# Kernel tuning notes

Hardware: AMD Instinct MI355X
Metric: run time of the kernel (lower is better)

Reference implementation:

```python
import math
import jax, jax.numpy as jnp
import numpy as np
from jax import lax

N_HEADS = 8
FACTOR = 5


def _pos_emb(L, d):
    pos = jnp.arange(L, dtype=jnp.float32)[:, None]
    div = jnp.exp(jnp.arange(0, d, 2, dtype=jnp.float32) * (-math.log(10000.0) / d))
    pe = jnp.zeros((L, d), jnp.float32)
    pe = pe.at[:, 0::2].set(jnp.sin(pos * div))
    pe = pe.at[:, 1::2].set(jnp.cos(pos * div))
    return pe


def _circ_conv1d(x, w, b=None):
    # x: (B, L, Cin); w: torch conv1d weight (Cout, Cin, 3); circular padding=1
    xp = jnp.concatenate([x[:, -1:], x, x[:, :1]], axis=1)
    y = lax.conv_general_dilated(xp, jnp.transpose(w, (2, 1, 0)), (1,), 'VALID',
                                 dimension_numbers=('NWC', 'WIO', 'NWC'))
    return y + b if b is not None else y


def _ln(x, g, b, eps=1e-5):
    mu = x.mean(-1, keepdims=True)
    var = ((x - mu) ** 2).mean(-1, keepdims=True)
    return (x - mu) * lax.rsqrt(var + eps) * g + b


def _prob_attn(q, k, v, key):
    # q,k,v: (b, h, L, d); self-attention so l_q == l_k == L
    b, h, L, d = q.shape
    u = min(L, int(FACTOR * math.log(L + 1)))  # sample_k == n_top
    idx = jnp.asarray(jax.random.randint(key, (L, u), 0, L))  # shared across b,h as in torch

    # sampled QK scores: scan over the u samples to avoid a (b,h,L,u,d) gather blow-up
    def step(_, idx_s):
        kg = k[:, :, idx_s]  # (b,h,L,d): key idx_s[l] for query l
        return None, jnp.einsum('bhld,bhld->bhl', q, kg)
    _, qk = lax.scan(step, None, idx.T)  # (u, b, h, L)
    qk = jnp.moveaxis(qk, 0, -1)  # (b, h, L, u)

    m = qk.max(axis=-1) - qk.mean(axis=-1)  # sparsity measure, (b,h,L)
    _, top = lax.top_k(m, u)  # (b,h,u) top-u query indices

    q_red = jnp.take_along_axis(q, top[..., None], axis=2)  # (b,h,u,d)
    scores = jnp.einsum('bhud,bhkd->bhuk', q_red, k) * (1.0 / math.sqrt(d))
    attn = jax.nn.softmax(scores, axis=-1)
    ctx_top = jnp.einsum('bhuk,bhkd->bhud', attn, v)

    # non-selected queries get mean(V); scatter sparse-attention rows back in
    ctx = jnp.broadcast_to(v.mean(axis=2, keepdims=True), (b, h, L, d))
    bi = jnp.arange(b)[:, None, None]
    hi = jnp.arange(h)[None, :, None]
    return ctx.at[bi, hi, top].set(ctx_top)


def _attn_layer(x, wq, bq, wk, bk, wv, bv, wo, bo, key):
    b, L, dm = x.shape
    dh = dm // N_HEADS
    def split(w_, b_):
        return (x @ w_.T + b_).reshape(b, L, N_HEADS, dh).transpose(0, 2, 1, 3)
    ctx = _prob_attn(split(wq, bq), split(wk, bk), split(wv, bv), key)
    ctx = ctx.transpose(0, 2, 1, 3).reshape(b, L, dm)
    return ctx @ wo.T + bo


def _conv_layer(x, w, b, g, beta):
    # circular conv -> BatchNorm (batch stats, train-mode math) -> ELU -> maxpool k3 s2 p1
    y = _circ_conv1d(x, w, b)
    mu = y.mean(axis=(0, 1))
    var = y.var(axis=(0, 1))
    y = (y - mu) * lax.rsqrt(var + 1e-5) * g + beta
    y = jax.nn.elu(y)
    yp = jnp.pad(y, ((0, 0), (1, 1), (0, 0)), constant_values=-np.inf)
    return lax.reduce_window(yp, -np.inf, lax.max, (1, 3, 1), (1, 2, 1), 'VALID')


def _forward(x, skip_w, skip_b, token_conv_w, wq, bq, wk, bk, wv, bv, wo, bo,
             w1, b1, w2, b2, ln1_g, ln1_b, ln2_g, ln2_b,
             dc_w, dc_b, bn_g, bn_b, final_ln_g, final_ln_b, proj_w, proj_b):
    skip = x[:, -1] @ skip_w.T + skip_b  # (B, pred_len)
    h = _circ_conv1d(x, token_conv_w)  # token embedding (no bias)
    h = h + _pos_emb(h.shape[1], h.shape[2])
    E = wq.shape[0]
    base = jax.random.key(42)
    for i in range(E):
        new_h = _attn_layer(h, wq[i], bq[i], wk[i], bk[i], wv[i], bv[i], wo[i], bo[i],
                            jax.random.fold_in(base, i))
        h = h + new_h
        y = _ln(h, ln1_g[i], ln1_b[i])
        y = jax.nn.gelu(y @ w1[i].T + b1[i], approximate=False)  # conv1 is 1x1
        y = y @ w2[i].T + b2[i]  # conv2 is 1x1
        h = _ln(h + y, ln2_g[i], ln2_b[i])
        if i < E - 1:
            h = _conv_layer(h, dc_w[i], dc_b[i], bn_g[i], bn_b[i])  # halves L
    h = _ln(h, final_ln_g, final_ln_b)
    return h[:, -1] @ proj_w.T + proj_b + skip


def setup_inputs() -> dict:
    B, L, C_IN, D, DFF, E, P = 32, 2048, 7, 512, 2048, 3, 96
    key = jax.random.key(0)
    ks = iter(jax.random.split(key, 20))
    w = lambda shape: jax.random.normal(next(ks), shape, jnp.float32) * 0.02
    z = lambda shape: jnp.zeros(shape, jnp.float32)
    o = lambda shape: jnp.ones(shape, jnp.float32)
    return {
        'x': jax.random.normal(next(ks), (B, L, C_IN), jnp.float32),
        'skip_w': w((P, C_IN)), 'skip_b': z((P,)),
        'token_conv_w': w((D, C_IN, 3)),
        'wq': w((E, D, D)), 'bq': z((E, D)),
        'wk': w((E, D, D)), 'bk': z((E, D)),
        'wv': w((E, D, D)), 'bv': z((E, D)),
        'wo': w((E, D, D)), 'bo': z((E, D)),
        'w1': w((E, DFF, D)), 'b1': z((E, DFF)),
        'w2': w((E, D, DFF)), 'b2': z((E, D)),
        'ln1_g': o((E, D)), 'ln1_b': z((E, D)),
        'ln2_g': o((E, D)), 'ln2_b': z((E, D)),
        'dc_w': w((E - 1, D, D, 3)), 'dc_b': z((E - 1, D)),
        'bn_g': o((E - 1, D)), 'bn_b': z((E - 1, D)),
        'final_ln_g': o((D,)), 'final_ln_b': z((D,)),
        'proj_w': w((P, D)), 'proj_b': z((P,)),
    }


def reference(x, skip_w, skip_b, token_conv_w, wq, bq, wk, bk, wv, bv, wo, bo,
              w1, b1, w2, b2, ln1_g, ln1_b, ln2_g, ln2_b,
              dc_w, dc_b, bn_g, bn_b, final_ln_g, final_ln_b, proj_w, proj_b):
    return _forward(x, skip_w, skip_b, token_conv_w, wq, bq, wk, bk, wv, bv, wo, bo,
                    w1, b1, w2, b2, ln1_g, ln1_b, ln2_g, ln2_b,
                    dc_w, dc_b, bn_g, bn_b, final_ln_g, final_ln_b, proj_w, proj_b)
```

## Files before the change

### kernel.cpp

```cpp
#include <hip/hip_runtime.h>
#include <cmath>

#define DM 512
#define DH 64

typedef __attribute__((ext_vector_type(8))) short short8;
typedef __attribute__((ext_vector_type(4))) float float4v;

__device__ inline float b2f(unsigned short u){
  union{unsigned int i; float f;} z; z.i = ((unsigned)u)<<16; return z.f;
}
__device__ inline unsigned short f2b(float f){
  unsigned int x = __float_as_uint(f);
  return (unsigned short)((x + 0x7fffu + ((x>>16)&1u)) >> 16);
}

#define GLL(gp, lp) __builtin_amdgcn_global_load_lds((const __attribute__((address_space(1))) void*)(gp), \
    (__attribute__((address_space(3))) void*)(lp), 16, 0, 0)

__host__ __device__ inline void tf2x32(unsigned k0, unsigned k1, unsigned& x0, unsigned& x1){
  const unsigned ks0=k0, ks1=k1, ks2=k0^k1^0x1BD11BDAu;
  x0 += ks0; x1 += ks1;
#define TF_ROT(r) { x0 += x1; x1 = (x1<<(r))|(x1>>(32-(r))); x1 ^= x0; }
  TF_ROT(13) TF_ROT(15) TF_ROT(26) TF_ROT(6)
  x0 += ks1; x1 += ks2 + 1u;
  TF_ROT(17) TF_ROT(29) TF_ROT(16) TF_ROT(24)
  x0 += ks2; x1 += ks0 + 2u;
  TF_ROT(13) TF_ROT(15) TF_ROT(26) TF_ROT(6)
  x0 += ks0; x1 += ks1 + 3u;
  TF_ROT(17) TF_ROT(29) TF_ROT(16) TF_ROT(24)
  x0 += ks1; x1 += ks2 + 4u;
  TF_ROT(13) TF_ROT(15) TF_ROT(26) TF_ROT(6)
  x0 += ks2; x1 += ks0 + 5u;
#undef TF_ROT
}

__global__ __launch_bounds__(256) void idx_kernel(int* __restrict__ idx, unsigned k2a, unsigned k2b,
                                                  int S2, int Lmask){
  int j = blockIdx.x*256 + threadIdx.x;
  if (j >= S2) return;
  unsigned x0 = (unsigned)j, x1 = (unsigned)(S2 + j);
  tf2x32(k2a, k2b, x0, x1);
  idx[j]      = (int)(x0 & (unsigned)Lmask);
  idx[S2 + j] = (int)(x1 & (unsigned)Lmask);
}

__global__ __launch_bounds__(256) void pe_kernel(float* __restrict__ pe, int L){
  int i = blockIdx.x*256 + threadIdx.x;
  int d = i % DM, l = i / DM;
  const float scale = -0.017988946f;
  float freq = expf((float)(d & ~1) * scale);
  float ang  = (float)l * freq;
  pe[i] = (d & 1) ? cosf(ang) : sinf(ang);
}

__global__ __launch_bounds__(256) void packtcw(const float* __restrict__ tcw, float* __restrict__ tcwT){
  int i = blockIdx.x*256 + threadIdx.x;
  if (i >= 21*DM) return;
  int j = i / DM, d = i % DM;
  tcwT[(size_t)j*DM + d] = tcw[(size_t)d*21 + (j%7)*3 + (j/7)];
}

__global__ __launch_bounds__(256) void embed2(const float* __restrict__ x, const float* __restrict__ tcwT,
                                              const float* __restrict__ pe, float* __restrict__ h, int L){
  int row = blockIdx.x; int l = row % L, b = row / L;
  __shared__ float xs[21];
  int t = threadIdx.x;
  if (t < 21){
    int c = t % 7, kk = t / 7;
    int ls = l + kk - 1; ls = (ls < 0) ? ls + L : (ls >= L ? ls - L : ls);
    xs[t] = x[((size_t)b*L + ls)*7 + c];
  }
  __syncthreads();
  for (int d = t; d < DM; d += 256){
    float acc = 0.f;
#pragma unroll
    for (int j=0;j<21;j++) acc += xs[j]*tcwT[j*DM + d];
    h[(size_t)row*DM + d] = acc + pe[(size_t)l*DM + d];
  }
}

__global__ __launch_bounds__(256) void f2b_vec(const float* __restrict__ src, unsigned short* __restrict__ dst, int n4){
  int i = blockIdx.x*256 + threadIdx.x;
  if (i >= n4) return;
  float4 v = ((const float4*)src)[i];
  ushort4 o; o.x = f2b(v.x); o.y = f2b(v.y); o.z = f2b(v.z); o.w = f2b(v.w);
  ((ushort4*)dst)[i] = o;
}

__global__ __launch_bounds__(256) void packconv(const float* __restrict__ dcw, unsigned short* __restrict__ wtapK){
  int i = blockIdx.x*256 + threadIdx.x;
  if (i >= 3*DM*DM) return;
  int n = i / (3*DM); int rem = i % (3*DM); int tap = rem / DM; int c = rem % DM;
  wtapK[(size_t)n*(3*DM) + tap*DM + c] = f2b(dcw[((size_t)n*DM + c)*3 + tap]);
}

__global__ __launch_bounds__(256) void catb_kernel(const float* __restrict__ a, const float* __restrict__ b,
    const float* __restrict__ c, float* __restrict__ o){
  int i = blockIdx.x*256 + threadIdx.x;
  if (i >= 1536) return;
  o[i] = (i < 512) ? a[i] : (i < 1024 ? b[i-512] : c[i-1024]);
}

template<int TN, int A32>
__global__ __launch_bounds__(256) void bgemm2(const void* __restrict__ Ain,
    const unsigned short* __restrict__ Wb, const float* __restrict__ bias, void* __restrict__ C,
    int N, int K, int L, int convmode, int act, int outbf, int qkv, size_t bufstride, int swz){
  constexpr int NJ = TN/32;
  constexpr int BR = TN/32;
  __shared__ unsigned short As[128*64];
  __shared__ unsigned short Bs[TN*64];
  int tid = threadIdx.x;
  int w = tid >> 6, ln = tid & 63;

  int bx = blockIdx.x, by = blockIdx.y;
  if (swz){
    int XT = gridDim.x, YT = gridDim.y;
    int lid = by*XT + bx;
    int xcd = lid & 7, s = lid >> 3;
    int ych = YT >> 3;
    int CHv = ych < 16 ? ych : 16;
    int yloc = s % CHv;
    int t2 = s / CHv;
    int xx = t2 % XT;
    int chunk = t2 / XT;
    by = xcd*ych + chunk*CHv + yloc;
    bx = xx;
  }
  int row0 = by*128, col0 = bx*TN;
  int KA = convmode ? 512 : K;

  long aBase[4], dPrev[4], dNext[4]; int aCol[4];
#pragma unroll
  for (int g=0; g<4; g++){
    int ch = g*256 + tid;
    int r = ch >> 3, c = ch & 7;
    int gc = c ^ (r & 7);
    int gr = row0 + r;
    aCol[g] = gc*8;
    aBase[g] = (long)gr * KA;
    if (convmode){
      int l = gr % L;
      dPrev[g] = (l==0)   ? (long)(L-1)*KA : -(long)KA;
      dNext[g] = (l==L-1) ? -(long)(L-1)*KA : (long)KA;
    } else { dPrev[g]=0; dNext[g]=0; }
  }
  long bBase[BR];
#pragma unroll
  for (int g=0; g<BR; g++){
    int ch = g*256 + tid;
    int r = ch >> 3, c = ch & 7;
    int gc = c ^ (r & 7);
    bBase[g] = (long)(col0 + r)*K + gc*8;
  }
  int raBase[4], rbBase[NJ];
#pragma unroll
  for (int i=0;i<4;i++)  raBase[i] = ((w&1)*64 + i*16 + (ln&15))*8;
#pragma unroll
  for (int j=0;j<NJ;j++) rbBase[j] = ((w>>1)*(TN/2) + j*16 + (ln&15))*8;

  float4v acc[4][NJ] = {};
  int nIter = K/64;
  const unsigned short* A16 = (const unsigned short*)Ain;
  const float* Af = (const float*)Ain;

  for (int it=0; it<nIter; it++){
    int k0 = it*64;
    int kk = convmode ? (k0 & 511) : k0;
    int seg = convmode ? (k0 >> 9) : 1;
    if (A32){
#pragma unroll
      for (int g=0; g<4; g++){
        long d = convmode ? ((seg==0) ? dPrev[g] : (seg==2 ? dNext[g] : 0)) : 0;
        const float* src = Af + aBase[g] + d + kk + aCol[g];
        float4 v0 = *(const float4*)src;
        float4 v1 = *(const float4*)(src+4);
        short8 pk;
        pk[0]=(short)f2b(v0.x); pk[1]=(short)f2b(v0.y); pk[2]=(short)f2b(v0.z); pk[3]=(short)f2b(v0.w);
        pk[4]=(short)f2b(v1.x); pk[5]=(short)f2b(v1.y); pk[6]=(short)f2b(v1.z); pk[7]=(short)f2b(v1.w);
        *(short8*)((char*)As + g*4096 + tid*16) = pk;
      }
    } else {
#pragma unroll
      for (int g=0; g<4; g++){
        long d = convmode ? ((seg==0) ? dPrev[g] : (seg==2 ? dNext[g] : 0)) : 0;
        GLL(A16 + aBase[g] + d + kk + aCol[g], (char*)As + g*4096 + w*1024);
      }
    }
#pragma unroll
    for (int g=0; g<BR; g++)
      GLL(Wb + bBase[g] + k0, (char*)Bs + g*4096 + w*1024);
    __syncthreads();
    const char* ab = (const char*)As;
    const char* bb = (const char*)Bs;
#pragma unroll
    for (int s=0;s<2;s++){
      int xs = (s*4 + (ln>>4)) ^ (ln&7);
      short8 af[4], bf[NJ];
#pragma unroll
      for (int i=0;i<4;i++)  af[i] = *(const short8*)(ab + (raBase[i] + xs)*16);
#pragma unroll
      for (int j=0;j<NJ;j++) bf[j] = *(const short8*)(bb + (rbBase[j] + xs)*16);
#pragma unroll
      for (int i=0;i<4;i++)
#pragma unroll
        for (int j=0;j<NJ;j++)
          acc[i][j] = __builtin_amdgcn_mfma_f32_16x16x32_bf16(af[i], bf[j], acc[i][j], 0, 0, 0);
    }
    __syncthreads();
  }

  float* Cf = (float*)C;
  unsigned short* Cb = (unsigned short*)C;
  int colb0 = col0 + (w>>1)*(TN/2) + (ln & 15);
#pragma unroll
  for (int i=0;i<4;i++){
#pragma unroll
    for (int r=0;r<4;r++){
      int grow = row0 + (w&1)*64 + i*16 + (ln>>4)*4 + r;
#pragma unroll
      for (int j=0;j<NJ;j++){
        int colb = colb0 + j*16;
        float v = acc[i][j][r];
        if (bias) v += bias[colb];
        if (act){
          float z = 0.7978845608f * v * (1.f + 0.044715f*v*v);
          float e = __expf(2.f*z);
          v = v * (1.f - 1.f/(e + 1.f));
        }
        if (outbf){
          if (qkv){
            int bsel = colb >> 9;
            Cb[(size_t)bsel*bufstride + (size_t)grow*512 + (colb & 511)] = f2b(v);
          } else {
            Cb[(size_t)grow*N + colb] = f2b(v);
          }
        } else {
          Cf[(size_t)grow*N + colb] = v;
        }
      }
    }
  }
}

__global__ __launch_bounds__(256) void sample_m2(const unsigned short* __restrict__ q,
    const unsigned short* __restrict__ k, const int* __restrict__ idx, float* __restrict__ m, int L, int u){
  int w = (blockIdx.x*256 + threadIdx.x) >> 6;
  int lane = threadIdx.x & 63;
  int l = w % L; int b = w / L;
  const unsigned short* qrow = q + (size_t)w*DM + lane*8;
  uint4 qq = *(const uint4*)qrow;
  float qv[8];
  qv[0]=b2f((unsigned short)(qq.x&0xffff)); qv[1]=b2f((unsigned short)(qq.x>>16));
  qv[2]=b2f((unsigned short)(qq.y&0xffff)); qv[3]=b2f((unsigned short)(qq.y>>16));
  qv[4]=b2f((unsigned short)(qq.z&0xffff)); qv[5]=b2f((unsigned short)(qq.z>>16));
  qv[6]=b2f((unsigned short)(qq.w&0xffff)); qv[7]=b2f((unsigned short)(qq.w>>16));
  const unsigned short* kb = k + (size_t)b*L*DM + lane*8;
  const int* ip = idx + (size_t)l*u;
  float mx = -1e30f, sum = 0.f;
  for (int s=0; s<u; s++){
    int kp = ip[s];
    uint4 kk = *(const uint4*)(kb + (size_t)kp*DM);
    float p;
    p  = qv[0]*b2f((unsigned short)(kk.x&0xffff)) + qv[1]*b2f((unsigned short)(kk.x>>16));
    p += qv[2]*b2f((unsigned short)(kk.y&0xffff)) + qv[3]*b2f((unsigned short)(kk.y>>16));
    p += qv[4]*b2f((unsigned short)(kk.z&0xffff)) + qv[5]*b2f((unsigned short)(kk.z>>16));
    p += qv[6]*b2f((unsigned short)(kk.w&0xffff)) + qv[7]*b2f((unsigned short)(kk.w>>16));
    p += __shfl_xor(p, 1); p += __shfl_xor(p, 2); p += __shfl_xor(p, 4);
    mx = fmaxf(mx, p); sum += p;
  }
  if ((lane & 7) == 0){
    int hh = lane >> 3;
    m[((size_t)b*8 + hh)*L + l] = mx - sum/(float)u;
  }
}

__global__ __launch_bounds__(256) void topk_kernel(const float* __restrict__ m, int* __restrict__ top, int L, int u){
  int bh = blockIdx.x;
  const float* mm = m + (size_t)bh*L;
  __shared__ float vals[2048];
  __shared__ float rv[256];
  __shared__ int   ri[256];
  for (int i=threadIdx.x; i<L; i+=256) vals[i] = mm[i];
  __syncthreads();
  for (int it=0; it<u; it++){
    float bv = -1e30f; int bi = 0x7fffffff;
    for (int i=threadIdx.x; i<L; i+=256){
      float v = vals[i];
      if (v > bv || (v == bv && i < bi)) { bv = v; bi = i; }
    }
    rv[threadIdx.x] = bv; ri[threadIdx.x] = bi;
    __syncthreads();
    for (int s=128; s; s>>=1){
      if (threadIdx.x < s){
        float v = rv[threadIdx.x+s]; int i2 = ri[threadIdx.x+s];
        if (v > rv[threadIdx.x] || (v == rv[threadIdx.x] && i2 < ri[threadIdx.x])){
          rv[threadIdx.x] = v; ri[threadIdx.x] = i2;
        }
      }
      __syncthreads();
    }
    if (threadIdx.x == 0){ top[bh*u + it] = ri[0]; vals[ri[0]] = -1e31f; }
    __syncthreads();
  }
}

#define CMC 32
__global__ __launch_bounds__(256) void colmean1(const float* __restrict__ src, float* __restrict__ part, int L){
  int b = blockIdx.x, ch = blockIdx.y;
  int rpb = L / CMC;
  int t = threadIdx.x;
  const float* p = src + ((size_t)b*L + (size_t)ch*rpb)*DM;
  float s0 = 0.f, s1 = 0.f;
  for (int r=0; r<rpb; r++){ s0 += p[(size_t)r*DM + t]; s1 += p[(size_t)r*DM + t + 256]; }
  float* o = part + ((size_t)b*CMC + ch)*DM;
  o[t] = s0; o[t+256] = s1;
}
__global__ __launch_bounds__(256) void colmean2(const float* __restrict__ part, float* __restrict__ dst, int L){
  int i = blockIdx.x*256 + threadIdx.x;
  int d = i % DM, b = i / DM;
  float s = 0.f;
  for (int c=0; c<CMC; c++) s += part[((size_t)b*CMC + c)*DM + d];
  dst[i] = s / (float)L;
}

__global__ __launch_bounds__(256) void tiny_gemm(const float* __restrict__ A, const float* __restrict__ W,
    const float* __restrict__ bias, float* __restrict__ C, int N, int K){
  int row = blockIdx.x;
  const float* ar = A + (size_t)row*K;
  __shared__ float as[DM];
  for (int k=threadIdx.x; k<K; k+=256) as[k] = ar[k];
  __syncthreads();
  for (int n = threadIdx.x; n < N; n += 256){
    float acc = bias ? bias[n] : 0.f;
    const float* wr = W + (size_t)n*K;
    for (int k=0; k<K; k++) acc += as[k]*wr[k];
    C[(size_t)row*N + n] = acc;
  }
}

__global__ __launch_bounds__(256) void qred_kernel(const unsigned short* __restrict__ q, const int* __restrict__ top,
    float* __restrict__ qred, int L, int u, int n){
  int i = blockIdx.x*256 + threadIdx.x;
  if (i >= n) return;
  int d = i & 63; int rest = i >> 6; int j = rest % u; int bh = rest / u;
  int hh = bh & 7; int b = bh >> 3;
  int pos = top[bh*u + j];
  qred[i] = b2f(q[((size_t)b*L + pos)*DM + hh*DH + d]);
}

#define FKT 128
__global__ __launch_bounds__(256) void flash_attn(const float* __restrict__ qred,
    const unsigned short* __restrict__ kbuf, const unsigned short* __restrict__ vbuf,
    float* __restrict__ partM, float* __restrict__ partL, float* __restrict__ partA,
    int L, int u, int KS){
  int ks = blockIdx.x, bh = blockIdx.y; int b = bh >> 3, h = bh & 7;
  int t = threadIdx.x;
  __shared__ float Qs[38*64];
  __shared__ unsigned short Ks[FKT*64];
  __shared__ unsigned short Vs[FKT*64];
  __shared__ float Ss[38*FKT];
  for (int i=t;i<u*64;i+=256) Qs[i] = qred[(size_t)bh*u*64 + i];
  int lane = t & 63, w = t >> 6;
  float rm[10], rl[10], racc[10];
#pragma unroll
  for (int j=0;j<10;j++){ rm[j]=-1e30f; rl[j]=0.f; racc[j]=0.f; }
  int nk = L / KS;
  int kbase = ks*nk;
  int key = t & 127, rh = t >> 7;
  for (int kt = 0; kt < nk; kt += FKT){
    __syncthreads();
    for (int e = t; e < FKT*8; e += 256){
      int k = e >> 3, c = e & 7;
      size_t gidx = ((size_t)(b*L + kbase + kt + k))*DM + h*DH + c*8;
      *(uint4*)((char*)Ks + (size_t)(k*8 + (c ^ (k&7)))*16) = *(const uint4*)(kbuf + gidx);
      *(uint4*)((char*)Vs + (size_t)e*16) = *(const uint4*)(vbuf + gidx);
    }
    __syncthreads();
    for (int r = rh; r < u; r += 2){
      const float4* q4 = (const float4*)(Qs + r*64);
      float acc = 0.f;
#pragma unroll
      for (int c=0;c<8;c++){
        short8 kk = *(const short8*)((char*)Ks + (size_t)(key*8 + (c ^ (key&7)))*16);
        float4 qa = q4[c*2], qb = q4[c*2+1];
        acc += qa.x*b2f((unsigned short)kk[0]) + qa.y*b2f((unsigned short)kk[1])
             + qa.z*b2f((unsigned short)kk[2]) + qa.w*b2f((unsigned short)kk[3]);
        acc += qb.x*b2f((unsigned short)kk[4]) + qb.y*b2f((unsigned short)kk[5])
             + qb.z*b2f((unsigned short)kk[6]) + qb.w*b2f((unsigned short)kk[7]);
      }
      Ss[r*FKT + key] = acc * 0.125f;
    }
    __syncthreads();
    int j = 0;
    for (int r = w; r < u; r += 4, j++){
      float s0 = Ss[r*FKT + lane], s1 = Ss[r*FKT + 64 + lane];
      float mx = fmaxf(s0, s1);
#pragma unroll
      for (int off=32; off; off>>=1) mx = fmaxf(mx, __shfl_xor(mx, off));
      float newm = fmaxf(rm[j], mx);
      float scale = expf(rm[j] - newm);
      float p0 = expf(s0 - newm), p1 = expf(s1 - newm);
      float ps = p0 + p1;
#pragma unroll
      for (int off=32; off; off>>=1) ps += __shfl_xor(ps, off);
      rl[j] = rl[j]*scale + ps;
      rm[j] = newm;
      Ss[r*FKT + lane] = p0; Ss[r*FKT + 64 + lane] = p1;
      float a = racc[j]*scale;
      for (int k=0;k<FKT;k+=4){
        float pa = Ss[r*FKT+k], pb = Ss[r*FKT+k+1], pc = Ss[r*FKT+k+2], pd = Ss[r*FKT+k+3];
        a += pa*b2f(Vs[(k+0)*64+lane]) + pb*b2f(Vs[(k+1)*64+lane])
           + pc*b2f(Vs[(k+2)*64+lane]) + pd*b2f(Vs[(k+3)*64+lane]);
      }
      racc[j] = a;
    }
  }
  int j = 0;
  for (int r = w; r < u; r += 4, j++){
    size_t base = ((size_t)bh*KS + ks)*u + r;
    if (lane == 0){ partM[base] = rm[j]; partL[base] = rl[j]; }
    partA[base*64 + lane] = racc[j];
  }
}

__global__ __launch_bounds__(256) void flash_merge(const float* __restrict__ partM, const float* __restrict__ partL,
    const float* __restrict__ partA, float* __restrict__ ctxt, int u, int KS, int n){
  int i = blockIdx.x*256 + threadIdx.x;
  if (i >= n) return;
  int nn = i & 63; int rest = i >> 6; int r = rest % u; int bhl = rest / u;
  size_t base0 = ((size_t)bhl*KS)*u + r;
  float gm = -1e30f;
  for (int s=0;s<KS;s++) gm = fmaxf(gm, partM[base0 + (size_t)s*u]);
  float lt = 0.f, at = 0.f;
  for (int s=0;s<KS;s++){
    float e = expf(partM[base0 + (size_t)s*u] - gm);
    lt += partL[base0 + (size_t)s*u]*e;
    at += partA[(base0 + (size_t)s*u)*64 + nn]*e;
  }
  ctxt[i] = at / lt;
}

__global__ __launch_bounds__(256) void scatter_delta(const float* __restrict__ ctxt, const float* __restrict__ vmean,
    const float* __restrict__ wo, const int* __restrict__ top, float* __restrict__ h, int L, int u){
  int bid = blockIdx.x;
  int j = bid % u; int bh = bid / u; int hh = bh & 7; int b = bh >> 3;
  int pos = top[bh*u + j];
  __shared__ float delta[DH];
  int t = threadIdx.x;
  if (t < DH) delta[t] = ctxt[(size_t)(bh*u + j)*DH + t] - vmean[b*DM + hh*DH + t];
  __syncthreads();
  float* hrow = h + ((size_t)b*L + pos)*DM;
  const float* wbase = wo + hh*DH;
  for (int n = t; n < DM; n += 256){
    float acc = 0.f;
    const float* wr = wbase + (size_t)n*DM;
#pragma unroll
    for (int dd=0; dd<DH; dd++) acc += delta[dd] * wr[dd];
    atomicAdd(&hrow[n], acc);
  }
}

__global__ __launch_bounds__(256) void ln_kernel(const float* __restrict__ X, const void* __restrict__ Yadd,
    int yb, const float* __restrict__ g, const float* __restrict__ bta, void* __restrict__ Out, int ob,
    const float* __restrict__ cwv, int Lrow, int row0g){
  size_t row = blockIdx.x;
  const float* xr = X + row*DM;
  int t = threadIdx.x;
  float v0 = xr[t], v1 = xr[t+256];
  if (cwv){
    int b = (int)((row0g + (int)row) / Lrow);
    v0 += cwv[b*DM + t]; v1 += cwv[b*DM + t+256];
  }
  if (Yadd){
    if (yb){ const unsigned short* yr = (const unsigned short*)Yadd + row*DM; v0 += b2f(yr[t]); v1 += b2f(yr[t+256]); }
    else   { const float* yr = (const float*)Yadd + row*DM; v0 += yr[t]; v1 += yr[t+256]; }
  }
  float s = v0+v1, q = v0*v0+v1*v1;
#pragma unroll
  for (int off=32; off; off>>=1){ s += __shfl_xor(s,off); q += __shfl_xor(q,off); }
  __shared__ float ss[4], qq[4];
  int w = t >> 6;
  if ((t & 63) == 0){ ss[w] = s; qq[w] = q; }
  __syncthreads();
  s = ss[0]+ss[1]+ss[2]+ss[3]; q = qq[0]+qq[1]+qq[2]+qq[3];
  float mu  = s * (1.0f/DM);
  float var = q * (1.0f/DM) - mu*mu;
  float r = rsqrtf(var + 1e-5f);
  float o0 = (v0 - mu)*r*g[t]     + bta[t];
  float o1 = (v1 - mu)*r*g[t+256] + bta[t+256];
  if (ob){
    unsigned short* Ob = (unsigned short*)Out;
    Ob[row*DM + t] = f2b(o0); Ob[row*DM + t+256] = f2b(o1);
  } else {
    float* Of = (float*)Out;
    Of[row*DM + t] = o0; Of[row*DM + t+256] = o1;
  }
}

__global__ __launch_bounds__(256) void bnstat1(const unsigned short* __restrict__ C, float* __restrict__ partS,
                                               float* __restrict__ partQ, int rpb){
  int chb = blockIdx.x;
  int mb  = blockIdx.y;
  int g = threadIdx.x >> 6, c = threadIdx.x & 63;
  int ch = chb*64 + c;
  float s = 0.f, q = 0.f;
  int r0 = mb * rpb;
  for (int r = r0 + g; r < r0 + rpb; r += 4){
    float v = b2f(C[(size_t)r*DM + ch]); s += v; q += v*v;
  }
  __shared__ float ls[4][64], lq[4][64];
  ls[g][c] = s; lq[g][c] = q;
  __syncthreads();
  if (g == 0){
    s = ls[0][c]+ls[1][c]+ls[2][c]+ls[3][c];
    q = lq[0][c]+lq[1][c]+lq[2][c]+lq[3][c];
    partS[(size_t)mb*DM + ch] = s;
    partQ[(size_t)mb*DM + ch] = q;
  }
}
__global__ __launch_bounds__(256) void bnstat2(const float* __restrict__ partS, const float* __restrict__ partQ,
                                               float* __restrict__ stats, int NB, int M){
  int ch = blockIdx.x*256 + threadIdx.x;
  if (ch >= DM) return;
  float s = 0.f, q = 0.f;
  for (int mb=0; mb<NB; mb++){
    s += partS[(size_t)mb*DM + ch];
    q += partQ[(size_t)mb*DM + ch];
  }
  float mu = s / (float)M;
  stats[ch] = mu;
  stats[DM + ch] = q / (float)M - mu*mu;
}

__global__ __launch_bounds__(256) void bnpool(const unsigned short* __restrict__ C, const float* __restrict__ stats,
    const float* __restrict__ g, const float* __restrict__ bta, float* __restrict__ Out,
    int L, int Lo){
  size_t i = (size_t)blockIdx.x*256 + threadIdx.x;
  int ch = (int)(i % DM);
  size_t r = i / DM;
  int lo = (int)(r % Lo);
  int b  = (int)(r / Lo);
  float mu = stats[ch];
  float rstd = rsqrtf(stats[DM+ch] + 1e-5f);
  float gg = g[ch], bb = bta[ch];
  float best = -1e30f;
#pragma unroll
  for (int t=-1; t<=1; t++){
    int li = 2*lo + t;
    if (li >= 0 && li < L){
      float v = (b2f(C[((size_t)b*L + li)*DM + ch]) - mu)*rstd*gg + bb;
      v = v > 0.f ? v : expm1f(v);
      best = fmaxf(best, v);
    }
  }
  Out[((size_t)b*Lo + lo)*DM + ch] = best;
}

__global__ __launch_bounds__(128) void final_kernel(const float* __restrict__ h, const float* __restrict__ x,
    const float* __restrict__ fg, const float* __restrict__ fb, const float* __restrict__ pw,
    const float* __restrict__ pb, const float* __restrict__ sw, const float* __restrict__ sb,
    float* __restrict__ out, int Lf, int L0){
  int b = blockIdx.x;
  const float* row = h + ((size_t)b*Lf + (Lf-1))*DM;
  __shared__ float xn[DM];
  __shared__ float rs[2], rq[2];
  int t = threadIdx.x;
  float v[4]; float s = 0.f, q = 0.f;
#pragma unroll
  for (int i=0;i<4;i++){ v[i] = row[t + i*128]; s += v[i]; q += v[i]*v[i]; }
#pragma unroll
  for (int off=32; off; off>>=1){ s += __shfl_xor(s,off); q += __shfl_xor(q,off); }
  if ((t & 63) == 0){ rs[t>>6] = s; rq[t>>6] = q; }
  __syncthreads();
  s = rs[0]+rs[1]; q = rq[0]+rq[1];
  float mu = s*(1.0f/DM), var = q*(1.0f/DM) - mu*mu;
  float r = rsqrtf(var + 1e-5f);
#pragma unroll
  for (int i=0;i<4;i++){ int d = t + i*128; xn[d] = (v[i]-mu)*r*fg[d] + fb[d]; }
  __syncthreads();
  if (t < 96){
    float acc = pb[t] + sb[t];
    const float* xr = x + ((size_t)b*L0 + (L0-1))*7;
#pragma unroll
    for (int c=0;c<7;c++) acc += xr[c]*sw[t*7+c];
    for (int d=0; d<DM; d++) acc += xn[d]*pw[(size_t)t*DM + d];
    out[b*96 + t] = acc;
  }
}

extern "C" void kernel_launch(void* const* d_in, const int* in_sizes, int n_in,
                              void* d_out, int out_size, void* d_ws, size_t ws_size,
                              hipStream_t stream){
  const float* x    = (const float*)d_in[0];
  const float* skw  = (const float*)d_in[1];
  const float* skb  = (const float*)d_in[2];
  const float* tcw  = (const float*)d_in[3];
  const float* wq   = (const float*)d_in[4];
  const float* bq   = (const float*)d_in[5];
  const float* wk   = (const float*)d_in[6];
  const float* bk   = (const float*)d_in[7];
  const float* wv   = (const float*)d_in[8];
  const float* bv   = (const float*)d_in[9];
  const float* wo   = (const float*)d_in[10];
  const float* bo   = (const float*)d_in[11];
  const float* w1   = (const float*)d_in[12];
  const float* b1   = (const float*)d_in[13];
  const float* w2   = (const float*)d_in[14];
  const float* b2   = (const float*)d_in[15];
  const float* ln1g = (const float*)d_in[16];
  const float* ln1b = (const float*)d_in[17];
  const float* ln2g = (const float*)d_in[18];
  const float* ln2b = (const float*)d_in[19];
  const float* dcw  = (const float*)d_in[20];
  const float* dcb  = (const float*)d_in[21];
  const float* bng  = (const float*)d_in[22];
  const float* bnb  = (const float*)d_in[23];
  const float* flg  = (const float*)d_in[24];
  const float* flb  = (const float*)d_in[25];
  const float* pw   = (const float*)d_in[26];
  const float* pb   = (const float*)d_in[27];

  const int B = 32, L0 = 2048, DFF = 2048;
  const int RG = 16384;
  const int RF = 8192;
  char* ws = (char*)d_ws;
  const size_t SZH  = (size_t)B*L0*DM*sizeof(float);
  const size_t SLOT = (size_t)RG*DM*sizeof(unsigned short);

  const size_t WBSZ = (size_t)(3*DM*DM + 2*DFF*DM + 3*DM*DM)*2;
  size_t small_bytes = (size_t)L0*40*4
                     + (size_t)RG*8*4
                     + (size_t)B*8*40*4
                     + (size_t)32*8*40*64*4
                     + (size_t)32*8*40*64*4
                     + 3*(size_t)B*DM*4
                     + 2*(size_t)128*DM*4
                     + (size_t)2*DM*4
                     + (size_t)1536*4
                     + (size_t)B*CMC*DM*4
                     + (size_t)L0*DM*4
                     + (size_t)21*DM*4;
  if (ws_size < SZH + 4*SLOT + WBSZ + small_bytes) return;

  float*          h   = (float*)(ws);
  unsigned short* P0  = (unsigned short*)(ws + SZH);
  unsigned short* P1  = (unsigned short*)(ws + SZH + SLOT);
  unsigned short* P2  = (unsigned short*)(ws + SZH + 2*SLOT);
  unsigned short* P3  = (unsigned short*)(ws + SZH + 3*SLOT);
  unsigned short* wb  = (unsigned short*)(ws + SZH + 4*SLOT);
  unsigned short* wqb = wb;
  unsigned short* w1b = wqb + (size_t)3*DM*DM;
  unsigned short* w2b = w1b + (size_t)DFF*DM;
  unsigned short* wtapK= w2b + (size_t)DM*DFF;
  char* sm = ws + SZH + 4*SLOT + WBSZ;
  int*   idx_buf  = (int*)sm;
  float* m_buf    = (float*)(sm + (size_t)L0*40*4);
  int*   top_all  = (int*)((char*)m_buf + (size_t)RG*8*4);
  float* qred_loc = (float*)((char*)top_all + (size_t)B*8*40*4);
  float* ctxt_all = qred_loc + (size_t)32*8*40*64;
  float* hm       = ctxt_all + (size_t)32*8*40*64;
  float* vmean    = hm + (size_t)B*DM;
  float* cw       = vmean + (size_t)B*DM;
  float* partS    = cw + (size_t)B*DM;
  float* partQ    = partS + (size_t)128*DM;
  float* stats    = partQ + (size_t)128*DM;
  float* bqkv     = stats + (size_t)2*DM;
  float* partC    = bqkv + (size_t)1536;
  float* pe_buf   = partC + (size_t)B*CMC*DM;
  float* tcwT     = pe_buf + (size_t)L0*DM;

  float* fpM = (float*)P0;
  float* fpL = fpM + (size_t)256*40;
  float* fpA = fpL + (size_t)256*40;

  auto conv_b = [&](const float* src, unsigned short* dst, size_t n){
    f2b_vec<<<(int)((n/4 + 255)/256), 256, 0, stream>>>(src, dst, (int)(n/4));
  };

  pe_kernel<<<(int)(((size_t)L0*DM)/256), 256, 0, stream>>>(pe_buf, L0);
  packtcw<<<(21*DM + 255)/256, 256, 0, stream>>>(tcw, tcwT);
  embed2<<<B*L0, 256, 0, stream>>>(x, tcwT, pe_buf, h, L0);

  int L = L0;
  for (int layer = 0; layer < 3; layer++){
    int M = B * L;
    int u = (int)(5.0 * log((double)L + 1.0));
    int G = RG / L;
    int nG = M / RG;
    int KS = L / 512;
    const float* wv_i = wv + (size_t)layer*DM*DM;  const float* bv_i = bv + (size_t)layer*DM;
    const float* wo_i = wo + (size_t)layer*DM*DM;  const float* bo_i = bo + (size_t)layer*DM;
    const float* b1_i = b1 + (size_t)layer*DFF;
    const float* b2_i = b2 + (size_t)layer*DM;

    conv_b(wq + (size_t)layer*DM*DM, wqb,                    (size_t)DM*DM);
    conv_b(wk + (size_t)layer*DM*DM, wqb + (size_t)DM*DM,    (size_t)DM*DM);
    conv_b(wv_i,                     wqb + (size_t)2*DM*DM,  (size_t)DM*DM);
    conv_b(w1 + (size_t)layer*DFF*DM, w1b, (size_t)DFF*DM);
    conv_b(w2 + (size_t)layer*DM*DFF, w2b, (size_t)DM*DFF);
    catb_kernel<<<6, 256, 0, stream>>>(bq + (size_t)layer*DM, bk + (size_t)layer*DM, bv_i, bqkv);
    if (layer < 2)
      packconv<<<(3*DM*DM + 255)/256, 256, 0, stream>>>(dcw + (size_t)layer*DM*DM*3, wtapK);

    unsigned ka = 0u, kb2 = (unsigned)layer;
    tf2x32(0u, 42u, ka, kb2);
    unsigned a0 = 0u, a1 = 2u;  tf2x32(ka, kb2, a0, a1);
    unsigned c0 = 1u, c1 = 3u;  tf2x32(ka, kb2, c0, c1);
    int S2 = L * u / 2;
    idx_kernel<<<(S2 + 255)/256, 256, 0, stream>>>(idx_buf, a1, c1, S2, L-1);

    for (int g = 0; g < nG; g++){
      const float* hg = h + (size_t)g*RG*DM;
      bgemm2<128,1><<<dim3(12, RG/128), 256, 0, stream>>>(hg, wqb, bqkv, P1,
          1536, 512, L, 0, 0, 1, 1, (size_t)RG*DM, 1);
      sample_m2<<<RG/4, 256, 0, stream>>>(P1, P2, idx_buf, m_buf, L, u);
      int* top_g = top_all + (size_t)g*G*8*u;
      topk_kernel<<<G*8, 256, 0, stream>>>(m_buf, top_g, L, u);
      int nqr = G*8*u*DH;
      qred_kernel<<<(nqr + 255)/256, 256, 0, stream>>>(P1, top_g, qred_loc, L, u, nqr);

      flash_attn<<<dim3(KS, G*8), 256, 0, stream>>>(qred_loc, P2, P3, fpM, fpL, fpA, L, u, KS);
      int nmg = G*8*u*64;
      flash_merge<<<(nmg + 255)/256, 256, 0, stream>>>(fpM, fpL, fpA,
          ctxt_all + (size_t)g*G*8*u*64, u, KS, nmg);
    }

    colmean1<<<dim3(B, CMC), 256, 0, stream>>>(h, partC, L);
    colmean2<<<B*DM/256, 256, 0, stream>>>(partC, hm, L);
    tiny_gemm<<<B, 256, 0, stream>>>(hm, wv_i, bv_i, vmean, DM, DM);
    tiny_gemm<<<B, 256, 0, stream>>>(vmean, wo_i, bo_i, cw, DM, DM);

    scatter_delta<<<B*8*u, 256, 0, stream>>>(ctxt_all, vmean, wo_i, top_all, h, L, u);

    unsigned short* ybuf = P0;
    unsigned short* mid  = P1;
    unsigned short* y2b  = P0 + (size_t)RF*DM;
    const float* l1g = ln1g + (size_t)layer*DM; const float* l1b = ln1b + (size_t)layer*DM;
    const float* l2g = ln2g + (size_t)layer*DM; const float* l2b = ln2b + (size_t)layer*DM;
    for (int r0 = 0; r0 < M; r0 += RF){
      ln_kernel<<<RF, 256, 0, stream>>>(h + (size_t)r0*DM, nullptr, 0, l1g, l1b, ybuf, 1, cw, L, r0);
      bgemm2<128,0><<<dim3(16, RF/128), 256, 0, stream>>>(ybuf, w1b, b1_i, mid,
          2048, 512, L, 0, 1, 1, 0, 0, 1);
      bgemm2<64,0><<<dim3(8, RF/128), 256, 0, stream>>>(mid, w2b, b2_i, y2b,
          512, 2048, L, 0, 0, 1, 0, 0, 1);
      ln_kernel<<<RF, 256, 0, stream>>>(h + (size_t)r0*DM, y2b, 1, l2g, l2b, h + (size_t)r0*DM, 0, cw, L, r0);
    }

    if (layer < 2){
      const float* db = dcb + (size_t)layer*DM;
      unsigned short* convb = P0;
      bgemm2<64,1><<<dim3(8, M/128), 256, 0, stream>>>(h, wtapK, db, convb,
          512, 1536, L, 1, 0, 1, 0, 0, 1);
      bnstat1<<<dim3(8, 128), 256, 0, stream>>>(convb, partS, partQ, M/128);
      bnstat2<<<2, 256, 0, stream>>>(partS, partQ, stats, 128, M);
      int Lo = L/2;
      bnpool<<<(int)(((size_t)B*Lo*DM)/256), 256, 0, stream>>>(convb, stats,
          bng + (size_t)layer*DM, bnb + (size_t)layer*DM, h, L, Lo);
      L = Lo;
    }
  }

  final_kernel<<<B, 128, 0, stream>>>(h, x, flg, flb, pw, pb, skw, skb, (float*)d_out, L, L0);
}
```

Measured before the change: 5.406 ms.

## Use packed bf16 conversion, register top-k, wave-per-row layernorm, wider conv tile

Swaps the software float-to-bf16 rounding for the hardware v_cvt_pk_bf16_f32 instruction in the conversion, GEMM staging and epilogue paths. The top-k kernel now keeps scores in registers and reduces with wave shuffles instead of an LDS tree with many barriers. LayerNorm processes one row per wave with vectorized loads and stores and no shared-memory reduction. The conv GEMM switches to a 128-wide N tile. The top-k kernel assumes L is a multiple of 256 and at most 2048, and the hardware conversion's rounding may differ slightly from the old software routine for special values.

```diff
diff --git a/kernel.cpp b/kernel.cpp
--- a/kernel.cpp
+++ b/kernel.cpp
@@ -13,6 +13,9 @@
 __device__ inline unsigned short f2b(float f){
   unsigned int x = __float_as_uint(f);
   return (unsigned short)((x + 0x7fffu + ((x>>16)&1u)) >> 16);
+}
+__device__ inline unsigned cvtpk2(float a, float b){
+  unsigned r; asm("v_cvt_pk_bf16_f32 %0, %1, %2" : "=v"(r) : "v"(a), "v"(b)); return r;
 }
 
 #define GLL(gp, lp) __builtin_amdgcn_global_load_lds((const __attribute__((address_space(1))) void*)(gp), \
@@ -84,8 +87,8 @@
   int i = blockIdx.x*256 + threadIdx.x;
   if (i >= n4) return;
   float4 v = ((const float4*)src)[i];
-  ushort4 o; o.x = f2b(v.x); o.y = f2b(v.y); o.z = f2b(v.z); o.w = f2b(v.w);
-  ((ushort4*)dst)[i] = o;
+  uint2 o; o.x = cvtpk2(v.x, v.y); o.y = cvtpk2(v.z, v.w);
+  ((uint2*)dst)[i] = o;
 }
 
 __global__ __launch_bounds__(256) void packconv(const float* __restrict__ dcw, unsigned short* __restrict__ wtapK){
@@ -175,10 +178,10 @@
         const float* src = Af + aBase[g] + d + kk + aCol[g];
         float4 v0 = *(const float4*)src;
         float4 v1 = *(const float4*)(src+4);
-        short8 pk;
-        pk[0]=(short)f2b(v0.x); pk[1]=(short)f2b(v0.y); pk[2]=(short)f2b(v0.z); pk[3]=(short)f2b(v0.w);
-        pk[4]=(short)f2b(v1.x); pk[5]=(short)f2b(v1.y); pk[6]=(short)f2b(v1.z); pk[7]=(short)f2b(v1.w);
-        *(short8*)((char*)As + g*4096 + tid*16) = pk;
+        uint4 pk;
+        pk.x = cvtpk2(v0.x, v0.y); pk.y = cvtpk2(v0.z, v0.w);
+        pk.z = cvtpk2(v1.x, v1.y); pk.w = cvtpk2(v1.z, v1.w);
+        *(uint4*)((char*)As + g*4096 + tid*16) = pk;
       }
     } else {
 #pragma unroll
@@ -215,12 +218,13 @@
   int colb0 = col0 + (w>>1)*(TN/2) + (ln & 15);
 #pragma unroll
   for (int i=0;i<4;i++){
-#pragma unroll
-    for (int r=0;r<4;r++){
-      int grow = row0 + (w&1)*64 + i*16 + (ln>>4)*4 + r;
-#pragma unroll
-      for (int j=0;j<NJ;j++){
-        int colb = colb0 + j*16;
+    int growb = row0 + (w&1)*64 + i*16 + (ln>>4)*4;
+#pragma unroll
+    for (int j=0;j<NJ;j++){
+      int colb = colb0 + j*16;
+      float vv[4];
+#pragma unroll
+      for (int r=0;r<4;r++){
         float v = acc[i][j][r];
         if (bias) v += bias[colb];
         if (act){
@@ -228,16 +232,29 @@
           float e = __expf(2.f*z);
           v = v * (1.f - 1.f/(e + 1.f));
         }
-        if (outbf){
-          if (qkv){
-            int bsel = colb >> 9;
-            Cb[(size_t)bsel*bufstride + (size_t)grow*512 + (colb & 511)] = f2b(v);
-          } else {
-            Cb[(size_t)grow*N + colb] = f2b(v);
-          }
+        vv[r] = v;
+      }
+      if (outbf){
+        unsigned p01 = cvtpk2(vv[0], vv[1]);
+        unsigned p23 = cvtpk2(vv[2], vv[3]);
+        unsigned short h0 = (unsigned short)p01, h1 = (unsigned short)(p01>>16);
+        unsigned short h2 = (unsigned short)p23, h3 = (unsigned short)(p23>>16);
+        if (qkv){
+          int bsel = colb >> 9;
+          size_t base = (size_t)bsel*bufstride + (colb & 511);
+          Cb[base + (size_t)(growb+0)*512] = h0;
+          Cb[base + (size_t)(growb+1)*512] = h1;
+          Cb[base + (size_t)(growb+2)*512] = h2;
+          Cb[base + (size_t)(growb+3)*512] = h3;
         } else {
-          Cf[(size_t)grow*N + colb] = v;
+          Cb[(size_t)(growb+0)*N + colb] = h0;
+          Cb[(size_t)(growb+1)*N + colb] = h1;
+          Cb[(size_t)(growb+2)*N + colb] = h2;
+          Cb[(size_t)(growb+3)*N + colb] = h3;
         }
+      } else {
+#pragma unroll
+        for (int r=0;r<4;r++) Cf[(size_t)(growb+r)*N + colb] = vv[r];
       }
     }
   }
@@ -275,32 +292,42 @@
   }
 }
 
+template<int NS>
 __global__ __launch_bounds__(256) void topk_kernel(const float* __restrict__ m, int* __restrict__ top, int L, int u){
   int bh = blockIdx.x;
   const float* mm = m + (size_t)bh*L;
-  __shared__ float vals[2048];
-  __shared__ float rv[256];
-  __shared__ int   ri[256];
-  for (int i=threadIdx.x; i<L; i+=256) vals[i] = mm[i];
-  __syncthreads();
+  int t = threadIdx.x;
+  float v[NS];
+#pragma unroll
+  for (int s=0; s<NS; s++) v[s] = mm[s*256 + t];
+  __shared__ float rv[4];
+  __shared__ int   ri[4];
   for (int it=0; it<u; it++){
     float bv = -1e30f; int bi = 0x7fffffff;
-    for (int i=threadIdx.x; i<L; i+=256){
-      float v = vals[i];
-      if (v > bv || (v == bv && i < bi)) { bv = v; bi = i; }
-    }
-    rv[threadIdx.x] = bv; ri[threadIdx.x] = bi;
+#pragma unroll
+    for (int s=0; s<NS; s++){
+      float x = v[s]; int i = s*256 + t;
+      if (x > bv || (x == bv && i < bi)) { bv = x; bi = i; }
+    }
+#pragma unroll
+    for (int off=32; off; off>>=1){
+      float ov = __shfl_xor(bv, off); int oi = __shfl_xor(bi, off);
+      if (ov > bv || (ov == bv && oi < bi)) { bv = ov; bi = oi; }
+    }
+    if ((t & 63) == 0){ rv[t>>6] = bv; ri[t>>6] = bi; }
     __syncthreads();
-    for (int s=128; s; s>>=1){
-      if (threadIdx.x < s){
-        float v = rv[threadIdx.x+s]; int i2 = ri[threadIdx.x+s];
-        if (v > rv[threadIdx.x] || (v == rv[threadIdx.x] && i2 < ri[threadIdx.x])){
-          rv[threadIdx.x] = v; ri[threadIdx.x] = i2;
-        }
-      }
-      __syncthreads();
-    }
-    if (threadIdx.x == 0){ top[bh*u + it] = ri[0]; vals[ri[0]] = -1e31f; }
+    bv = rv[0]; bi = ri[0];
+#pragma unroll
+    for (int k2=1; k2<4; k2++){
+      float ov = rv[k2]; int oi = ri[k2];
+      if (ov > bv || (ov == bv && oi < bi)) { bv = ov; bi = oi; }
+    }
+    if (t == 0) top[bh*u + it] = bi;
+    if ((bi & 255) == t){
+      int slot = bi >> 8;
+#pragma unroll
+      for (int s=0; s<NS; s++) if (s == slot) v[s] = -1e31f;
+    }
     __syncthreads();
   }
 }
@@ -464,37 +491,60 @@
 __global__ __launch_bounds__(256) void ln_kernel(const float* __restrict__ X, const void* __restrict__ Yadd,
     int yb, const float* __restrict__ g, const float* __restrict__ bta, void* __restrict__ Out, int ob,
     const float* __restrict__ cwv, int Lrow, int row0g){
-  size_t row = blockIdx.x;
-  const float* xr = X + row*DM;
-  int t = threadIdx.x;
-  float v0 = xr[t], v1 = xr[t+256];
+  int w = threadIdx.x >> 6, lane = threadIdx.x & 63;
+  size_t row = (size_t)blockIdx.x*4 + w;
+  int d0 = lane*8;
+  const float* xr = X + row*DM + d0;
+  float4 a = *(const float4*)xr;
+  float4 b = *(const float4*)(xr+4);
+  float v[8] = {a.x,a.y,a.z,a.w,b.x,b.y,b.z,b.w};
   if (cwv){
-    int b = (int)((row0g + (int)row) / Lrow);
-    v0 += cwv[b*DM + t]; v1 += cwv[b*DM + t+256];
+    int bb = (int)(((size_t)row0g + row) / (size_t)Lrow);
+    const float* cp = cwv + (size_t)bb*DM + d0;
+    float4 c0 = *(const float4*)cp, c1 = *(const float4*)(cp+4);
+    v[0]+=c0.x; v[1]+=c0.y; v[2]+=c0.z; v[3]+=c0.w;
+    v[4]+=c1.x; v[5]+=c1.y; v[6]+=c1.z; v[7]+=c1.w;
   }
   if (Yadd){
-    if (yb){ const unsigned short* yr = (const unsigned short*)Yadd + row*DM; v0 += b2f(yr[t]); v1 += b2f(yr[t+256]); }
-    else   { const float* yr = (const float*)Yadd + row*DM; v0 += yr[t]; v1 += yr[t+256]; }
-  }
-  float s = v0+v1, q = v0*v0+v1*v1;
+    if (yb){
+      const unsigned short* yr = (const unsigned short*)Yadd + row*DM + d0;
+      uint4 yv = *(const uint4*)yr;
+      v[0]+=b2f((unsigned short)(yv.x&0xffff)); v[1]+=b2f((unsigned short)(yv.x>>16));
+      v[2]+=b2f((unsigned short)(yv.y&0xffff)); v[3]+=b2f((unsigned short)(yv.y>>16));
+      v[4]+=b2f((unsigned short)(yv.z&0xffff)); v[5]+=b2f((unsigned short)(yv.z>>16));
+      v[6]+=b2f((unsigned short)(yv.w&0xffff)); v[7]+=b2f((unsigned short)(yv.w>>16));
+    } else {
+      const float* yr = (const float*)Yadd + row*DM + d0;
+      float4 y0 = *(const float4*)yr, y1 = *(const float4*)(yr+4);
+      v[0]+=y0.x; v[1]+=y0.y; v[2]+=y0.z; v[3]+=y0.w;
+      v[4]+=y1.x; v[5]+=y1.y; v[6]+=y1.z; v[7]+=y1.w;
+    }
+  }
+  float s = 0.f, q = 0.f;
+#pragma unroll
+  for (int i=0;i<8;i++){ s += v[i]; q += v[i]*v[i]; }
 #pragma unroll
   for (int off=32; off; off>>=1){ s += __shfl_xor(s,off); q += __shfl_xor(q,off); }
-  __shared__ float ss[4], qq[4];
-  int w = t >> 6;
-  if ((t & 63) == 0){ ss[w] = s; qq[w] = q; }
-  __syncthreads();
-  s = ss[0]+ss[1]+ss[2]+ss[3]; q = qq[0]+qq[1]+qq[2]+qq[3];
   float mu  = s * (1.0f/DM);
   float var = q * (1.0f/DM) - mu*mu;
   float r = rsqrtf(var + 1e-5f);
-  float o0 = (v0 - mu)*r*g[t]     + bta[t];
-  float o1 = (v1 - mu)*r*g[t+256] + bta[t+256];
+  const float* gp = g + d0; const float* bp = bta + d0;
+  float4 g0 = *(const float4*)gp, g1 = *(const float4*)(gp+4);
+  float4 b0 = *(const float4*)bp, b1 = *(const float4*)(bp+4);
+  float gg[8] = {g0.x,g0.y,g0.z,g0.w,g1.x,g1.y,g1.z,g1.w};
+  float bb2[8] = {b0.x,b0.y,b0.z,b0.w,b1.x,b1.y,b1.z,b1.w};
+  float o[8];
+#pragma unroll
+  for (int i=0;i<8;i++) o[i] = (v[i]-mu)*r*gg[i] + bb2[i];
   if (ob){
-    unsigned short* Ob = (unsigned short*)Out;
-    Ob[row*DM + t] = f2b(o0); Ob[row*DM + t+256] = f2b(o1);
+    uint4 pk;
+    pk.x = cvtpk2(o[0],o[1]); pk.y = cvtpk2(o[2],o[3]);
+    pk.z = cvtpk2(o[4],o[5]); pk.w = cvtpk2(o[6],o[7]);
+    *(uint4*)((unsigned short*)Out + row*DM + d0) = pk;
   } else {
-    float* Of = (float*)Out;
-    Of[row*DM + t] = o0; Of[row*DM + t+256] = o1;
+    float* Of = (float*)Out + row*DM + d0;
+    *(float4*)Of     = make_float4(o[0],o[1],o[2],o[3]);
+    *(float4*)(Of+4) = make_float4(o[4],o[5],o[6],o[7]);
   }
 }
 
@@ -716,7 +766,9 @@
           1536, 512, L, 0, 0, 1, 1, (size_t)RG*DM, 1);
       sample_m2<<<RG/4, 256, 0, stream>>>(P1, P2, idx_buf, m_buf, L, u);
       int* top_g = top_all + (size_t)g*G*8*u;
-      topk_kernel<<<G*8, 256, 0, stream>>>(m_buf, top_g, L, u);
+      if (L == 2048)      topk_kernel<8><<<G*8, 256, 0, stream>>>(m_buf, top_g, L, u);
+      else if (L == 1024) topk_kernel<4><<<G*8, 256, 0, stream>>>(m_buf, top_g, L, u);
+      else                topk_kernel<2><<<G*8, 256, 0, stream>>>(m_buf, top_g, L, u);
       int nqr = G*8*u*DH;
       qred_kernel<<<(nqr + 255)/256, 256, 0, stream>>>(P1, top_g, qred_loc, L, u, nqr);
 
@@ -739,18 +791,18 @@
     const float* l1g = ln1g + (size_t)layer*DM; const float* l1b = ln1b + (size_t)layer*DM;
     const float* l2g = ln2g + (size_t)layer*DM; const float* l2b = ln2b + (size_t)layer*DM;
     for (int r0 = 0; r0 < M; r0 += RF){
-      ln_kernel<<<RF, 256, 0, stream>>>(h + (size_t)r0*DM, nullptr, 0, l1g, l1b, ybuf, 1, cw, L, r0);
+      ln_kernel<<<RF/4, 256, 0, stream>>>(h + (size_t)r0*DM, nullptr, 0, l1g, l1b, ybuf, 1, cw, L, r0);
       bgemm2<128,0><<<dim3(16, RF/128), 256, 0, stream>>>(ybuf, w1b, b1_i, mid,
           2048, 512, L, 0, 1, 1, 0, 0, 1);
       bgemm2<64,0><<<dim3(8, RF/128), 256, 0, stream>>>(mid, w2b, b2_i, y2b,
           512, 2048, L, 0, 0, 1, 0, 0, 1);
-      ln_kernel<<<RF, 256, 0, stream>>>(h + (size_t)r0*DM, y2b, 1, l2g, l2b, h + (size_t)r0*DM, 0, cw, L, r0);
+      ln_kernel<<<RF/4, 256, 0, stream>>>(h + (size_t)r0*DM, y2b, 1, l2g, l2b, h + (size_t)r0*DM, 0, cw, L, r0);
     }
 
     if (layer < 2){
       const float* db = dcb + (size_t)layer*DM;
       unsigned short* convb = P0;
-      bgemm2<64,1><<<dim3(8, M/128), 256, 0, stream>>>(h, wtapK, db, convb,
+      bgemm2<128,1><<<dim3(4, M/128), 256, 0, stream>>>(h, wtapK, db, convb,
           512, 1536, L, 1, 0, 1, 0, 0, 1);
       bnstat1<<<dim3(8, 128), 256, 0, stream>>>(convb, partS, partQ, M/128);
       bnstat2<<<2, 256, 0, stream>>>(partS, partQ, stats, 128, M);
```

After: 4.959 ms. 1.09x faster.
